# Performance work log

Hardware: AMD Instinct MI355X
Metric: run time of the kernel (lower is better)

The kernel has to match this reference:

```python
import jax, jax.numpy as jnp
import numpy as np

B, T, D = 2, 4096, 1024
H = 16
KD, VD = 512, 1024          # expand_k=0.5, expand_v=1.0
HK, HV = KD // H, VD // H   # 32, 64
CHUNK = 64
GATE_RANK = 16
GATE_NORM = 16.0            # gate_logit_normalizer
EPS = 1e-5


def setup_inputs() -> dict:
    key = jax.random.key(0)
    ks = jax.random.split(key, 10)
    w = lambda k, shape: (jax.random.normal(k, shape, jnp.float32) * 0.02)
    return {
        "x":      jax.random.normal(ks[0], (B, T, D), jnp.float32),
        "Wq":     w(ks[1], (D, KD)),
        "Wk":     w(ks[2], (D, KD)),
        "Wv":     w(ks[3], (D, VD)),
        "Wgk1":   w(ks[4], (D, GATE_RANK)),
        "Wgk2":   w(ks[5], (GATE_RANK, KD)),
        "bgk":    jnp.zeros((KD,), jnp.float32),
        "Wg":     w(ks[6], (D, VD)),
        "norm_w": jnp.ones((HV,), jnp.float32),
        "Wo":     w(ks[7], (VD, D)),
    }


def _split_chunks(t, hd):
    # [B, T, H*hd] -> [nC, B, H, C, hd]
    nC = T // CHUNK
    t = t.reshape(B, nC, CHUNK, H, hd)
    return jnp.transpose(t, (1, 0, 3, 2, 4))


def reference(x, Wq, Wk, Wv, Wgk1, Wgk2, bgk, Wg, norm_w, Wo):
    scale = HK ** -0.5
    q = _split_chunks(x @ Wq, HK)                       # [nC,B,H,C,HK]
    k = _split_chunks(x @ Wk, HK)
    v = _split_chunks(x @ Wv, HV)                       # [nC,B,H,C,HV]
    gk = jax.nn.log_sigmoid((x @ Wgk1) @ Wgk2 + bgk) / GATE_NORM
    gk = _split_chunks(gk, HK)                          # [nC,B,H,C,HK]

    mask = jnp.tril(jnp.ones((CHUNK, CHUNK), bool))

    def step(S, inp):
        qc, kc, vc, gc = inp                            # [B,H,C,hk/hv]
        b = jnp.cumsum(gc, axis=2)                      # cumulative log-decay
        qe = qc * jnp.exp(b) * scale
        # intra-chunk causal attention with relative decay exp(b_i - b_j)
        A = jnp.einsum('bhik,bhjk->bhij', qe, kc * jnp.exp(-b))
        A = jnp.where(mask, A, 0.0)
        o = jnp.einsum('bhij,bhjv->bhiv', A, vc)
        # inter-chunk contribution from carried state
        o = o + jnp.einsum('bhik,bhkv->bhiv', qe, S)
        b_last = b[:, :, -1]                            # [B,H,hk]
        ke = kc * jnp.exp(b_last[:, :, None, :] - b)
        S = jnp.exp(b_last)[..., None] * S + jnp.einsum('bhjk,bhjv->bhkv', ke, vc)
        return S, o

    S0 = jnp.zeros((B, H, HK, HV), x.dtype)
    _, o = jax.lax.scan(step, S0, (q, k, v, gk))        # o: [nC,B,H,C,HV]
    o = jnp.transpose(o, (1, 0, 3, 2, 4)).reshape(B, T, H, HV)

    # fused gated RMSNorm (FusedRMSNormSwishGate) per head
    g = (x @ Wg).reshape(B, T, H, HV)
    rms = o * jax.lax.rsqrt(jnp.mean(o * o, axis=-1, keepdims=True) + EPS) * norm_w
    out = rms * (g * jax.nn.sigmoid(g))
    return out.reshape(B, T, VD) @ Wo
```

## Files before the change

kernel.cpp:

```cpp
#include <hip/hip_runtime.h>
#include <cstddef>

#define B_   2
#define T_   4096
#define D_   1024
#define H_   16
#define KD_  512
#define VD_  1024
#define NC_  64
#define M_   (B_*T_)
#define GR_  16
#define EPS_ 1e-5f
#define SCALE_ 0.17677669529663687f
#define GNORM_INV_ (1.0f/16.0f)

#define NF_   3200
#define Q0_   0
#define K0_   512
#define V0_   1024
#define G0_   2048
#define GL0_  3072

typedef __attribute__((ext_vector_type(8))) __bf16 bf16x8;
typedef __attribute__((ext_vector_type(4))) float f32x4;

__device__ inline unsigned short f2bf(float f) {
  unsigned int u = __float_as_uint(f);
  u = (u + 0x7fffu + ((u >> 16) & 1u)) >> 16;
  return (unsigned short)u;
}
__device__ inline float bf2f(unsigned short u) {
  return __uint_as_float((unsigned int)u << 16);
}
__device__ inline void unpack8(uint4 u, float* f) {
  f[0] = bf2f(u.x & 0xffff); f[1] = bf2f(u.x >> 16);
  f[2] = bf2f(u.y & 0xffff); f[3] = bf2f(u.y >> 16);
  f[4] = bf2f(u.z & 0xffff); f[5] = bf2f(u.z >> 16);
  f[6] = bf2f(u.w & 0xffff); f[7] = bf2f(u.w >> 16);
}
__device__ inline uint4 pack8(const unsigned short* s) {
  uint4 u;
  u.x = (unsigned int)s[0] | ((unsigned int)s[1] << 16);
  u.y = (unsigned int)s[2] | ((unsigned int)s[3] << 16);
  u.z = (unsigned int)s[4] | ((unsigned int)s[5] << 16);
  u.w = (unsigned int)s[6] | ((unsigned int)s[7] << 16);
  return u;
}

__device__ __forceinline__ void gload_lds16(const unsigned short* g, unsigned short* l) {
  __builtin_amdgcn_global_load_lds(
      (const __attribute__((address_space(1))) unsigned int*)g,
      (__attribute__((address_space(3))) unsigned int*)l, 16, 0, 0);
}


__global__ __launch_bounds__(256) void k_f32_to_bf16(const float* __restrict__ in,
                                                     unsigned short* __restrict__ out, int n4) {
  int i = (blockIdx.x * 256 + threadIdx.x) * 4;
  float4 f = *(const float4*)(in + i);
  ushort4 o;
  o.x = f2bf(f.x); o.y = f2bf(f.y); o.z = f2bf(f.z); o.w = f2bf(f.w);
  *(ushort4*)(out + i) = o;
}

__global__ __launch_bounds__(256) void k_transpose_all(const float* __restrict__ Wq,
                                                       const float* __restrict__ Wk,
                                                       const float* __restrict__ Wv,
                                                       const float* __restrict__ Wg,
                                                       const float* __restrict__ Wo,
                                                       const float* __restrict__ Wgk1,
                                                       unsigned short* __restrict__ Wcat,
                                                       unsigned short* __restrict__ woT) {
  __shared__ float tile[32][33];
  const float* in; unsigned short* out; int N;
  switch (blockIdx.z) {
    case 0: in = Wq;   out = Wcat + (size_t)Q0_ * D_;  N = 512;  break;
    case 1: in = Wk;   out = Wcat + (size_t)K0_ * D_;  N = 512;  break;
    case 2: in = Wv;   out = Wcat + (size_t)V0_ * D_;  N = 1024; break;
    case 3: in = Wg;   out = Wcat + (size_t)G0_ * D_;  N = 1024; break;
    case 4: in = Wo;   out = woT;                      N = 1024; break;
    default: in = Wgk1; out = Wcat + (size_t)GL0_ * D_; N = 128;  break;
  }
  int n0 = blockIdx.x * 32, k0 = blockIdx.y * 32;
  if (n0 >= N) return;
  int tx = threadIdx.x & 31, ty = threadIdx.x >> 5;
  if (blockIdx.z == 5) {
#pragma unroll
    for (int p = 0; p < 4; ++p)
      tile[ty + p*8][tx] = (n0 + tx < GR_) ? in[(size_t)(k0 + ty + p*8) * GR_ + n0 + tx] : 0.0f;
  } else {
#pragma unroll
    for (int p = 0; p < 4; ++p)
      tile[ty + p*8][tx] = in[(size_t)(k0 + ty + p*8) * N + n0 + tx];
  }
  __syncthreads();
#pragma unroll
  for (int p = 0; p < 4; ++p)
    out[(size_t)(n0 + ty + p*8) * 1024 + k0 + tx] = f2bf(tile[tx][ty + p*8]);
}


template <typename OutT>
__global__ __launch_bounds__(256, 3) void k_gemm_bt(const unsigned short* __restrict__ A,
                                                    const unsigned short* __restrict__ Bt,
                                                    OutT* __restrict__ C,
                                                    int M, int N, int K) {
  __shared__ __align__(16) unsigned short sA[128 * 64];
  __shared__ __align__(16) unsigned short sB[128 * 64];
  const int tid  = threadIdx.x;
  const int lane = tid & 63;
  const int wave = tid >> 6;
  const int wr = wave >> 1, wc = wave & 1;
  const int quad = lane >> 4, l16 = lane & 15;

  const int g = blockIdx.x;
  const int xcd = g & 7, slot = g >> 3;
  const int bm0 = ((xcd << 3) | (slot & 7)) << 7;
  const int bn0 = (slot >> 3) << 7;

  const int lrow = lane >> 3;
  const int gcol = ((lane & 7) ^ lrow) * 8;
  const unsigned short* ga = A  + (size_t)(bm0 + wave * 8 + lrow) * K + gcol;
  const unsigned short* gb = Bt + (size_t)(bn0 + wave * 8 + lrow) * K + gcol;
  unsigned short* la = sA + wave * 8 * 64;
  unsigned short* lb = sB + wave * 8 * 64;

  f32x4 acc[4][4] = {};

  for (int k0 = 0; k0 < K; k0 += 64) {
#pragma unroll
    for (int it = 0; it < 4; ++it) {
      gload_lds16(ga + k0 + (size_t)it * 32 * K, la + it * 32 * 64);
      gload_lds16(gb + k0 + (size_t)it * 32 * K, lb + it * 32 * 64);
    }
    __syncthreads();
#pragma unroll
    for (int kk = 0; kk < 2; ++kk) {
      bf16x8 af[4], bfv[4];
#pragma unroll
      for (int i = 0; i < 4; ++i) {
        int row = wr * 64 + i * 16 + l16;
        int gg = (kk * 4 + quad) ^ (row & 7);
        af[i] = *(const bf16x8*)(sA + row * 64 + gg * 8);
      }
#pragma unroll
      for (int j = 0; j < 4; ++j) {
        int row = wc * 64 + j * 16 + l16;
        int gg = (kk * 4 + quad) ^ (row & 7);
        bfv[j] = *(const bf16x8*)(sB + row * 64 + gg * 8);
      }
#pragma unroll
      for (int i = 0; i < 4; ++i)
#pragma unroll
        for (int j = 0; j < 4; ++j)
          acc[i][j] = __builtin_amdgcn_mfma_f32_16x16x32_bf16(af[i], bfv[j], acc[i][j], 0, 0, 0);
    }
    __syncthreads();
  }

#pragma unroll
  for (int i = 0; i < 4; ++i) {
    int row0 = bm0 + wr * 64 + i * 16 + quad * 4;
#pragma unroll
    for (int j = 0; j < 4; ++j) {
      int col = bn0 + wc * 64 + j * 16 + l16;
#pragma unroll
      for (int r = 0; r < 4; ++r) {
        float v = acc[i][j][r];
        if constexpr (sizeof(OutT) == 2)
          C[(size_t)(row0 + r) * N + col] = (OutT)f2bf(v);
        else
          C[(size_t)(row0 + r) * N + col] = (OutT)v;
      }
    }
  }
}


#define P1_SGLOW 0
#define P1_SW2   2048
#define P1_SBGK  4096
#define P1_QN    4224
#define P1_KN    9344
#define P1_VN    14464
#define P1_VT    23680
#define P1_QEA   32896
#define P1_KEB   38016
#define P1_KET   43136
#define P1_EBL   47744
#define P1_AL    P1_QN
#define P1_SIZE  47872

__global__ __launch_bounds__(256) void k_phase1(unsigned short* __restrict__ pbuf,
                                                const float* __restrict__ Wgk2,
                                                const float* __restrict__ bgk,
                                                unsigned short* __restrict__ obuf,
                                                unsigned short* __restrict__ Ut,
                                                float* __restrict__ dvec) {
  const int bi = blockIdx.x;
  const int c = bi >> 5, bh = bi & 31;
  const int b = bh >> 4, h = bh & 15;
  const int tid = threadIdx.x;
  const int lane = tid & 63, w = tid >> 6;
  const int quad = lane >> 4, l16 = lane & 15;

  __shared__ __align__(16) char sm[P1_SIZE];

  const size_t row0 = (size_t)(b * T_ + c * 64);
  const size_t rq  = row0 * NF_ + Q0_ + h * 32;
  const size_t rk  = row0 * NF_ + K0_ + h * 32;
  const size_t rv  = row0 * NF_ + V0_ + h * 64;
  const size_t rgl = row0 * NF_ + GL0_;
  const size_t cb  = (size_t)c * 32 + bh;

  {
    int i = tid >> 2, seg = tid & 3;
    uint4 qu = *(const uint4*)(pbuf + rq + (size_t)i * NF_ + seg * 8);
    uint4 ku = *(const uint4*)(pbuf + rk + (size_t)i * NF_ + seg * 8);
    *(uint4*)(sm + P1_QN + i * 80 + seg * 16) = qu;
    *(uint4*)(sm + P1_KN + i * 80 + seg * 16) = ku;
  }
#pragma unroll
  for (int s = 0; s < 2; ++s) {
    int e = tid + s * 256;
    int j = e >> 3, seg = e & 7;
    uint4 vu = *(const uint4*)(pbuf + rv + (size_t)j * NF_ + seg * 8);
    *(uint4*)(sm + P1_VN + j * 144 + seg * 16) = vu;
  }
  if (tid < 128) {
    int i = tid >> 1, seg = tid & 1;
    uint4 gu = *(const uint4*)(pbuf + rgl + (size_t)i * NF_ + seg * 8);
    *(uint4*)(sm + P1_SGLOW + i * 32 + seg * 16) = gu;
    int r = tid >> 3, d4 = (tid & 7) * 4;
    *(float4*)(sm + P1_SW2 + (r * 32 + d4) * 4) = *(const float4*)(Wgk2 + r * KD_ + h * 32 + d4);
  }
  if (tid < 8)
    *(float4*)(sm + P1_SBGK + tid * 16) = *(const float4*)(bgk + h * 32 + tid * 4);
  __syncthreads();

  {
    int vd = tid & 63, jg = tid >> 6;
#pragma unroll
    for (int half = 0; half < 2; ++half) {
      int j0 = jg * 8 + half * 32;
      unsigned short t8[8];
#pragma unroll
      for (int jj = 0; jj < 8; ++jj)
        t8[jj] = *(const unsigned short*)(sm + P1_VN + (j0 + jj) * 144 + vd * 2);
      *(uint4*)(sm + P1_VT + vd * 144 + j0 * 2) = pack8(t8);
    }
  }

  {
    const int i = lane, dg = w;
    float gl[16];
    unpack8(*(const uint4*)(sm + P1_SGLOW + i * 32), gl);
    unpack8(*(const uint4*)(sm + P1_SGLOW + i * 32 + 16), gl + 8);
    float s[8];
    {
      float4 b0 = *(const float4*)(sm + P1_SBGK + dg * 32);
      float4 b1 = *(const float4*)(sm + P1_SBGK + dg * 32 + 16);
      s[0] = b0.x; s[1] = b0.y; s[2] = b0.z; s[3] = b0.w;
      s[4] = b1.x; s[5] = b1.y; s[6] = b1.z; s[7] = b1.w;
    }
#pragma unroll
    for (int r = 0; r < 16; ++r) {
      float4 wa = *(const float4*)(sm + P1_SW2 + (r * 32 + dg * 8) * 4);
      float4 wb = *(const float4*)(sm + P1_SW2 + (r * 32 + dg * 8) * 4 + 16);
      float gv = gl[r];
      s[0] += gv * wa.x; s[1] += gv * wa.y; s[2] += gv * wa.z; s[3] += gv * wa.w;
      s[4] += gv * wb.x; s[5] += gv * wb.y; s[6] += gv * wb.z; s[7] += gv * wb.w;
    }
    float bb[8];
#pragma unroll
    for (int j = 0; j < 8; ++j) {
      float ls = fminf(s[j], 0.0f) - __logf(1.0f + __expf(-fabsf(s[j])));
      float v = ls * GNORM_INV_;
#pragma unroll
      for (int off = 1; off < 64; off <<= 1) {
        int src = lane - off;
        float t2 = __shfl(v, src < 0 ? 0 : src, 64);
        if (lane >= off) v += t2;
      }
      bb[j] = v;
    }
    if (lane == 63) {
#pragma unroll
      for (int j = 0; j < 8; ++j) {
        float e = __expf(bb[j]);
        ((float*)(sm + P1_EBL))[dg * 8 + j] = e;
        dvec[cb * 32 + dg * 8 + j] = e;
      }
    }
    float qf[8], kf[8];
    unpack8(*(const uint4*)(sm + P1_QN + i * 80 + dg * 16), qf);
    unpack8(*(const uint4*)(sm + P1_KN + i * 80 + dg * 16), kf);
    unsigned short qo[8], ko[8];
#pragma unroll
    for (int j = 0; j < 8; ++j) {
      float eb = __expf(bb[j]);
      float ie = __expf(-bb[j]);
      qo[j] = f2bf(qf[j] * eb * SCALE_);
      ko[j] = f2bf(kf[j] * ie);
      *(unsigned short*)(sm + P1_KET + (dg * 8 + j) * 144 + i * 2) = ko[j];
    }
    *(uint4*)(sm + P1_QEA + i * 80 + dg * 16) = pack8(qo);
    *(uint4*)(sm + P1_KEB + i * 80 + dg * 16) = pack8(ko);
  }
  __syncthreads();

  {
    int i = tid >> 2, seg = tid & 3;
    *(uint4*)(pbuf + rq + (size_t)i * NF_ + seg * 8) =
        *(const uint4*)(sm + P1_QEA + i * 80 + seg * 16);
  }

  const int tm = w;
  bf16x8 aq = *(const bf16x8*)(sm + P1_QEA + (tm * 16 + l16) * 80 + quad * 16);
  f32x4 cA[4] = {};
#pragma unroll
  for (int tn = 0; tn < 4; ++tn) {
    bf16x8 bk = *(const bf16x8*)(sm + P1_KEB + (tn * 16 + l16) * 80 + quad * 16);
    cA[tn] = __builtin_amdgcn_mfma_f32_16x16x32_bf16(aq, bk, cA[tn], 0, 0, 0);
  }

  {
    const int um = w >> 1;
    bf16x8 ak0 = *(const bf16x8*)(sm + P1_KET + (um * 16 + l16) * 144 + quad * 16);
    bf16x8 ak1 = *(const bf16x8*)(sm + P1_KET + (um * 16 + l16) * 144 + quad * 16 + 64);
    f32x4 cU[2] = {};
#pragma unroll
    for (int e = 0; e < 2; ++e) {
      int un = (w & 1) * 2 + e;
      bf16x8 bv0 = *(const bf16x8*)(sm + P1_VT + (un * 16 + l16) * 144 + quad * 16);
      bf16x8 bv1 = *(const bf16x8*)(sm + P1_VT + (un * 16 + l16) * 144 + quad * 16 + 64);
      cU[e] = __builtin_amdgcn_mfma_f32_16x16x32_bf16(ak0, bv0, cU[e], 0, 0, 0);
      cU[e] = __builtin_amdgcn_mfma_f32_16x16x32_bf16(ak1, bv1, cU[e], 0, 0, 0);
    }
#pragma unroll
    for (int e = 0; e < 2; ++e) {
      int un = (w & 1) * 2 + e;
#pragma unroll
      for (int r = 0; r < 4; ++r) {
        int d = um * 16 + quad * 4 + r;
        int vd = un * 16 + l16;
        float eb = ((const float*)(sm + P1_EBL))[d];
        Ut[cb * 2048 + vd * 32 + d] = f2bf(cU[e][r] * eb);
      }
    }
  }

#pragma unroll
  for (int tn = 0; tn < 4; ++tn)
#pragma unroll
    for (int r = 0; r < 4; ++r) {
      int row = tm * 16 + quad * 4 + r;
      int col = tn * 16 + l16;
      float av = (col <= row) ? cA[tn][r] : 0.0f;
      *(unsigned short*)(sm + P1_AL + row * 144 + col * 2) = f2bf(av);
    }
  __syncthreads();

  {
    bf16x8 aA0 = *(const bf16x8*)(sm + P1_AL + (tm * 16 + l16) * 144 + quad * 16);
    bf16x8 aA1 = *(const bf16x8*)(sm + P1_AL + (tm * 16 + l16) * 144 + quad * 16 + 64);
#pragma unroll
    for (int tn = 0; tn < 4; ++tn) {
      bf16x8 bv0 = *(const bf16x8*)(sm + P1_VT + (tn * 16 + l16) * 144 + quad * 16);
      bf16x8 bv1 = *(const bf16x8*)(sm + P1_VT + (tn * 16 + l16) * 144 + quad * 16 + 64);
      f32x4 co = {};
      co = __builtin_amdgcn_mfma_f32_16x16x32_bf16(aA0, bv0, co, 0, 0, 0);
      co = __builtin_amdgcn_mfma_f32_16x16x32_bf16(aA1, bv1, co, 0, 0, 0);
#pragma unroll
      for (int r = 0; r < 4; ++r) {
        int row = tm * 16 + quad * 4 + r;
        int col = tn * 16 + l16;
        obuf[cb * 4096 + row * 64 + col] = f2bf(co[r]);
      }
    }
  }
}


__global__ __launch_bounds__(128) void k_phase2(const unsigned short* __restrict__ Ut,
                                                const float* __restrict__ dvec,
                                                unsigned short* __restrict__ Sp) {
  int idx = blockIdx.x * 128 + threadIdx.x;
  int bh = idx >> 10, q = idx & 1023;
  int vd = q >> 4, d2 = (q & 15) * 2;
  float run0 = 0.0f, run1 = 0.0f;
  for (int c = 0; c < NC_; ++c) {
    size_t o = ((size_t)c * 32 + bh) * 2048 + vd * 32 + d2;
    unsigned int uu = *(const unsigned int*)(Ut + o);
    *(unsigned int*)(Sp + o) =
        (unsigned int)f2bf(run0) | ((unsigned int)f2bf(run1) << 16);
    float dv0 = dvec[((size_t)c * 32 + bh) * 32 + d2];
    float dv1 = dvec[((size_t)c * 32 + bh) * 32 + d2 + 1];
    run0 = dv0 * run0 + bf2f(uu & 0xffff);
    run1 = dv1 * run1 + bf2f(uu >> 16);
  }
}


#define P3_QEA 0
#define P3_SL  5120
#define P3_OL  10240
#define P3_SIZE 27648

__global__ __launch_bounds__(256) void k_phase3rms(const unsigned short* __restrict__ pbuf,
                                                   const unsigned short* __restrict__ obuf,
                                                   const unsigned short* __restrict__ Sp,
                                                   const float* __restrict__ norm_w,
                                                   unsigned short* __restrict__ ybuf) {
  const int bi = blockIdx.x;
  const int c = bi >> 5, bh = bi & 31;
  const int b = bh >> 4, h = bh & 15;
  const int tid = threadIdx.x;
  const int lane = tid & 63, w = tid >> 6;
  const int quad = lane >> 4, l16 = lane & 15;

  __shared__ __align__(16) char sm[P3_SIZE];

  const size_t row0 = (size_t)(b * T_ + c * 64);
  const size_t rq = row0 * NF_ + Q0_ + h * 32;
  const size_t cb = (size_t)c * 32 + bh;

  {
    int i = tid >> 2, seg = tid & 3;
    *(uint4*)(sm + P3_QEA + i * 80 + seg * 16) =
        *(const uint4*)(pbuf + rq + (size_t)i * NF_ + seg * 8);
    *(uint4*)(sm + P3_SL + i * 80 + seg * 16) =
        *(const uint4*)(Sp + cb * 2048 + (size_t)i * 32 + seg * 8);
  }
  __syncthreads();

  const int tm = w;
  bf16x8 aq = *(const bf16x8*)(sm + P3_QEA + (tm * 16 + l16) * 80 + quad * 16);
#pragma unroll
  for (int tn = 0; tn < 4; ++tn) {
    bf16x8 bs = *(const bf16x8*)(sm + P3_SL + (tn * 16 + l16) * 80 + quad * 16);
    f32x4 co = {};
    co = __builtin_amdgcn_mfma_f32_16x16x32_bf16(aq, bs, co, 0, 0, 0);
#pragma unroll
    for (int r = 0; r < 4; ++r) {
      int row = tm * 16 + quad * 4 + r;
      int col = tn * 16 + l16;
      float o = co[r] + bf2f(obuf[cb * 4096 + row * 64 + col]);
      *(float*)(sm + P3_OL + (row * 68 + col) * 4) = o;
    }
  }
  __syncthreads();

  {
    int r0 = tid >> 3, s8 = tid & 7;
#pragma unroll
    for (int half = 0; half < 2; ++half) {
      int row = r0 + half * 32;
      float4 a  = *(const float4*)(sm + P3_OL + (row * 68 + s8 * 8) * 4);
      float4 b4 = *(const float4*)(sm + P3_OL + (row * 68 + s8 * 8) * 4 + 16);
      float p = a.x*a.x + a.y*a.y + a.z*a.z + a.w*a.w
              + b4.x*b4.x + b4.y*b4.y + b4.z*b4.z + b4.w*b4.w;
      p += __shfl_xor(p, 1, 64);
      p += __shfl_xor(p, 2, 64);
      p += __shfl_xor(p, 4, 64);
      float rs = rsqrtf(p * (1.0f / 64.0f) + EPS_);
      size_t m = row0 + row;
      float gv[8];
      unpack8(*(const uint4*)(pbuf + m * NF_ + G0_ + h * 64 + s8 * 8), gv);
      float4 n0 = *(const float4*)(norm_w + s8 * 8);
      float4 n1 = *(const float4*)(norm_w + s8 * 8 + 4);
      float nw[8] = {n0.x, n0.y, n0.z, n0.w, n1.x, n1.y, n1.z, n1.w};
      float ov[8] = {a.x, a.y, a.z, a.w, b4.x, b4.y, b4.z, b4.w};
      unsigned short yo[8];
#pragma unroll
      for (int j = 0; j < 8; ++j) {
        float sw = gv[j] / (1.0f + __expf(-gv[j]));
        yo[j] = f2bf(ov[j] * rs * nw[j] * sw);
      }
      *(uint4*)(ybuf + m * VD_ + h * 64 + s8 * 8) = pack8(yo);
    }
  }
}


extern "C" void kernel_launch(void* const* d_in, const int* in_sizes, int n_in,
                              void* d_out, int out_size, void* d_ws, size_t ws_size,
                              hipStream_t stream) {
  const float* x    = (const float*)d_in[0];
  const float* Wq   = (const float*)d_in[1];
  const float* Wk   = (const float*)d_in[2];
  const float* Wv   = (const float*)d_in[3];
  const float* Wgk1 = (const float*)d_in[4];
  const float* Wgk2 = (const float*)d_in[5];
  const float* bgk  = (const float*)d_in[6];
  const float* Wg   = (const float*)d_in[7];
  const float* nw   = (const float*)d_in[8];
  const float* Wo   = (const float*)d_in[9];
  float* out = (float*)d_out;

  char* p = (char*)d_ws;
  unsigned short* xb   = (unsigned short*)p;  p += (size_t)M_ * D_ * 2;
  unsigned short* Wcat = (unsigned short*)p;  p += (size_t)NF_ * D_ * 2;
  unsigned short* woT  = (unsigned short*)p;  p += (size_t)D_ * VD_ * 2;
  unsigned short* pbuf = (unsigned short*)p;  p += (size_t)M_ * NF_ * 2;
  unsigned short* obuf = (unsigned short*)p;  p += (size_t)M_ * VD_ * 2;
  unsigned short* Ubuf = (unsigned short*)p;  p += (size_t)NC_ * 32 * 2048 * 2;
  unsigned short* Sbuf = (unsigned short*)p;  p += (size_t)NC_ * 32 * 2048 * 2;
  float* dbuf = (float*)p;                    p += (size_t)NC_ * 32 * 32 * 4;
  unsigned short* ybuf = (unsigned short*)p;  p += (size_t)M_ * VD_ * 2;

  k_f32_to_bf16<<<(M_ * D_ / 4) / 256, 256, 0, stream>>>(x, xb, M_ * D_);
  k_transpose_all<<<dim3(32, 32, 6), 256, 0, stream>>>(Wq, Wk, Wv, Wg, Wo, Wgk1, Wcat, woT);

  k_gemm_bt<unsigned short><<<(NF_/128) * (M_/128), 256, 0, stream>>>(xb, Wcat, pbuf, M_, NF_, D_);

  k_phase1<<<NC_ * 32, 256, 0, stream>>>(pbuf, Wgk2, bgk, obuf, Ubuf, dbuf);
  k_phase2<<<256, 128, 0, stream>>>(Ubuf, dbuf, Sbuf);
  k_phase3rms<<<NC_ * 32, 256, 0, stream>>>(pbuf, obuf, Sbuf, nw, ybuf);

  k_gemm_bt<float><<<(D_/128) * (M_/128), 256, 0, stream>>>(ybuf, woT, out, M_, D_, VD_);
}
```

Baseline: 243.8 us.

## Replace projection GEMM with 256x256 tiled, pipelined MFMA kernel and XCD swizzle

Swaps the 128x128 projection GEMM for a new 256x256-tile, 512-thread kernel. It uses direct global-to-LDS loads with XOR-swizzled layout, double buffering across K-steps, and interleaved MFMA phases with barriers and priority hints. Blocks are remapped across the eight XCDs. The fused output width is padded from 3200 to 3328 columns so it divides into 256-wide tiles, with the padding rows of the weight matrix zeroed by a memset. This costs about 4% extra compute and changes the pbuf row stride that downstream kernels index with NF_.

```diff
diff --git a/kernel.cpp b/kernel.cpp
--- a/kernel.cpp
+++ b/kernel.cpp
@@ -14,7 +14,8 @@
 #define SCALE_ 0.17677669529663687f
 #define GNORM_INV_ (1.0f/16.0f)
 
-#define NF_   3200
+#define NF_   3328
+#define NVALID_ 3200
 #define Q0_   0
 #define K0_   512
 #define V0_   1024
@@ -172,6 +173,130 @@
         else
           C[(size_t)(row0 + r) * N + col] = (OutT)v;
       }
+    }
+  }
+}
+
+
+#define SA_(BUF, COL)                                                              \
+  { char* d_ = smb + (BUF) * 65536 + stg;                                          \
+    gload_lds16(pa + (COL),                     (unsigned short*)(d_));            \
+    gload_lds16(pa + (COL) + (size_t)8 * Kv,    (unsigned short*)(d_ + 1024));     \
+    gload_lds16(pa + (COL) + (size_t)128 * Kv,  (unsigned short*)(d_ + 16384));    \
+    gload_lds16(pa + (COL) + (size_t)136 * Kv,  (unsigned short*)(d_ + 17408)); }
+
+#define SB_(BUF, COL)                                                              \
+  { char* d_ = smb + (BUF) * 65536 + 32768 + stg;                                  \
+    gload_lds16(pb + (COL),                     (unsigned short*)(d_));            \
+    gload_lds16(pb + (COL) + (size_t)8 * Kv,    (unsigned short*)(d_ + 1024));     \
+    gload_lds16(pb + (COL) + (size_t)128 * Kv,  (unsigned short*)(d_ + 16384));    \
+    gload_lds16(pb + (COL) + (size_t)136 * Kv,  (unsigned short*)(d_ + 17408)); }
+
+#define RD_A(QM, G0)                                                               \
+  _Pragma("unroll") for (int m_ = 0; m_ < 4; ++m_) {                               \
+    const int ra_ = (QM) * 64 + m_ * 16 + l16;                                     \
+    av[m_] = *(const bf16x8*)(smb + aRd + ra_ * 128 + (((G0) ^ (ra_ & 7)) * 16)); }
+
+#define RD_B(G0)                                                                   \
+  _Pragma("unroll") for (int n_ = 0; n_ < 4; ++n_) {                               \
+    const int rn_ = (wc & 1) * 64 + n_ * 16 + l16;                                 \
+    bv[n_] = *(const bf16x8*)(smb + bRd + rn_ * 128 + (((G0) ^ (rn_ & 7)) * 16)); }
+
+#define MM_(QM)                                                                    \
+  __builtin_amdgcn_s_barrier();                                                    \
+  asm volatile("s_waitcnt lgkmcnt(0)" ::: "memory");                               \
+  __builtin_amdgcn_sched_barrier(0);                                               \
+  __builtin_amdgcn_s_setprio(1);                                                   \
+  _Pragma("unroll") for (int n_ = 0; n_ < 4; ++n_)                                 \
+    _Pragma("unroll") for (int m_ = 0; m_ < 4; ++m_)                               \
+      acc[(QM)*4 + m_][n_] =                                                       \
+        __builtin_amdgcn_mfma_f32_16x16x32_bf16(av[m_], bv[n_], acc[(QM)*4 + m_][n_], 0, 0, 0); \
+  __builtin_amdgcn_s_setprio(0);
+
+#define TILE_(RB, SA_CODE, SB_CODE, WAIT_CODE)                                     \
+  { const int aRd = (RB) * 65536 + wr * 16384;                                     \
+    const int bRd = (RB) * 65536 + 32768 + (wc >> 1) * 16384;                      \
+                                \
+    RD_A(0, quad) RD_B(quad)                                                       \
+    SA_CODE                                                                        \
+    MM_(0)                                                                         \
+    __builtin_amdgcn_s_barrier();                                                  \
+                                                           \
+    RD_A(1, quad)                                                                  \
+    MM_(1)                                                                         \
+    __builtin_amdgcn_s_barrier();                                                  \
+                                                   \
+    RD_A(0, 4 + quad) RD_B(4 + quad)                                               \
+    MM_(0)                                                                         \
+    __builtin_amdgcn_s_barrier();                                                  \
+                            \
+    RD_A(1, 4 + quad)                                                              \
+    SB_CODE                                                                        \
+    MM_(1)                                                                         \
+    WAIT_CODE                                                                      \
+    __builtin_amdgcn_s_barrier(); }
+
+template <int Mv, int Nv, int Kv>
+__global__ __launch_bounds__(512, 2) void k_gemm256(const unsigned short* __restrict__ A,
+                                                    const unsigned short* __restrict__ Bt,
+                                                    unsigned short* __restrict__ C) {
+  constexpr int NT = Kv / 64;
+  constexpr int NWG = (Mv / 256) * (Nv / 256);
+  static_assert(NWG % 8 == 0, "grid must be divisible by 8 for the XCD swizzle");
+  __shared__ __align__(16) char smb[131072];
+
+  const int tid  = threadIdx.x;
+  const int lane = tid & 63;
+  const int wv   = tid >> 6;
+  const int wr   = wv >> 2;
+  const int wc   = wv & 3;
+  const int quad = lane >> 4, l16 = lane & 15;
+
+  const int g  = blockIdx.x;
+  const int wg = (g & 7) * (NWG / 8) + (g >> 3);
+  const int bm0 = (wg % (Mv / 256)) * 256;
+  const int bn0 = (wg / (Mv / 256)) * 256;
+
+  const int srow = lane >> 3;
+  const int scol = ((lane & 7) ^ srow) * 8;
+  const unsigned short* pa = A  + (size_t)(bm0 + wv * 16 + srow) * Kv + scol;
+  const unsigned short* pb = Bt + (size_t)(bn0 + wv * 16 + srow) * Kv + scol;
+  const unsigned stg = (unsigned)(wv * 2048);
+
+  bf16x8 av[4], bv[4];
+  f32x4 acc[8][4] = {};
+
+  SA_(0, 0)
+  SB_(0, 0)
+  SB_(1, 64)
+  asm volatile("s_waitcnt vmcnt(4)" ::: "memory");
+  __builtin_amdgcn_s_barrier();
+
+  size_t colA = 64, colB = 128;
+#pragma unroll 2
+  for (int s = 0; s < NT - 2; ++s) {
+    const int rb = s & 1;
+    TILE_(rb,
+          SA_((rb ^ 1), colA),
+          SB_(rb, colB),
+          asm volatile("s_waitcnt vmcnt(4)" ::: "memory");)
+    colA += 64; colB += 64;
+  }
+  TILE_(((NT - 2) & 1),
+        SA_(((NT - 1) & 1), colA),
+        ,
+        asm volatile("s_waitcnt vmcnt(0)" ::: "memory");)
+  TILE_(((NT - 1) & 1), , , )
+
+#pragma unroll
+  for (int mi = 0; mi < 8; ++mi) {
+    const int row0 = bm0 + wr * 128 + mi * 16 + quad * 4;
+#pragma unroll
+    for (int n = 0; n < 4; ++n) {
+      const int col = bn0 + wc * 64 + n * 16 + l16;
+#pragma unroll
+      for (int r = 0; r < 4; ++r)
+        C[(size_t)(row0 + r) * Nv + col] = f2bf(acc[mi][n][r]);
     }
   }
 }
@@ -509,10 +634,12 @@
   float* dbuf = (float*)p;                    p += (size_t)NC_ * 32 * 32 * 4;
   unsigned short* ybuf = (unsigned short*)p;  p += (size_t)M_ * VD_ * 2;
 
+  hipMemsetAsync(Wcat + (size_t)NVALID_ * D_, 0, (size_t)(NF_ - NVALID_) * D_ * 2, stream);
+
   k_f32_to_bf16<<<(M_ * D_ / 4) / 256, 256, 0, stream>>>(x, xb, M_ * D_);
   k_transpose_all<<<dim3(32, 32, 6), 256, 0, stream>>>(Wq, Wk, Wv, Wg, Wo, Wgk1, Wcat, woT);
 
-  k_gemm_bt<unsigned short><<<(NF_/128) * (M_/128), 256, 0, stream>>>(xb, Wcat, pbuf, M_, NF_, D_);
+  k_gemm256<M_, NF_, D_><<<(M_ / 256) * (NF_ / 256), 512, 0, stream>>>(xb, Wcat, pbuf);
 
   k_phase1<<<NC_ * 32, 256, 0, stream>>>(pbuf, Wgk2, bgk, obuf, Ubuf, dbuf);
   k_phase2<<<256, 128, 0, stream>>>(Ubuf, dbuf, Sbuf);
```

Result: no change. 243.1 us (-0.3%).
